# Performance work log

Hardware: AMD Instinct MI355X
Metric: run time of the kernel (lower is better)

Reference implementation:

```python
import jax, jax.numpy as jnp
import numpy as np

B, S, D, H, FF, L = 2, 2048, 512, 8, 2048, 2
HD = D // H
EPS = 1e-5
NEG = -1e9


def layernorm(x, gamma, beta):
    # mean/var over last axis (axis=2 in original)
    mean = jnp.mean(x, axis=-1, keepdims=True)
    var = jnp.mean((x - mean) ** 2, axis=-1, keepdims=True)
    return gamma * (x - mean) / jnp.sqrt(var + EPS) + beta


def masked_attention(x, mask, Wqkv, Wo, bo):
    b, s, d = x.shape
    qkv = x @ Wqkv                                  # [B,S,3D]
    qkv = qkv.reshape(b, s, H, 3 * HD)
    qkv = qkv.reshape(b, H, s, 3 * HD)              # original uses reshape, not transpose
    q, k, v = jnp.split(qkv, 3, axis=3)             # each [B,H,S,HD]
    scaled = jnp.einsum('bhqd,bhkd->bhqk', q, k) / (HD ** 0.5)
    col = mask[:, None, None, :]                    # valid key columns
    row = mask[:, None, :, None]                    # valid query rows
    logits = jnp.where(col, scaled, NEG)
    attn = jax.nn.softmax(logits, axis=-1)
    attn = attn * (row & col).astype(attn.dtype)    # exact zeros outside valid block
    values = jnp.einsum('bhqk,bhkd->bhqd', attn, v)  # [B,H,S,HD]
    values = values.reshape(b, s, H * HD)           # original uses reshape, not transpose
    return values @ Wo + bo


def encoder_layer(x, mask, p):
    res = x
    x = masked_attention(x, mask, p['Wqkv'], p['Wo'], p['bo'])
    x = layernorm(x + res, p['g1'], p['be1'])
    res = x
    x = jax.nn.relu(x @ p['W1'] + p['bf1']) @ p['W2'] + p['bf2']
    x = layernorm(x + res, p['g2'], p['be2'])
    return x


def setup_inputs() -> dict:
    key = jax.random.key(0)
    ks = jax.random.split(key, 8)
    x = jax.random.normal(ks[0], (B, S, D), jnp.float32)
    lengths = jax.random.randint(ks[1], (B,), S // 2, S + 1)
    paded_mask = jnp.arange(S)[None, :] < lengths[:, None]   # [B,S] bool
    sc = 0.02
    return {
        'x': x,
        'paded_mask': paded_mask,
        'Wqkv': jax.random.normal(ks[2], (L, D, 3 * D), jnp.float32) * sc,
        'Wo': jax.random.normal(ks[3], (L, D, D), jnp.float32) * sc,
        'bo': jnp.zeros((L, D), jnp.float32),
        'g1': jnp.ones((L, D), jnp.float32),
        'be1': jnp.zeros((L, D), jnp.float32),
        'W1': jax.random.normal(ks[4], (L, D, FF), jnp.float32) * sc,
        'bf1': jnp.zeros((L, FF), jnp.float32),
        'W2': jax.random.normal(ks[5], (L, FF, D), jnp.float32) * sc,
        'bf2': jnp.zeros((L, D), jnp.float32),
        'g2': jnp.ones((L, D), jnp.float32),
        'be2': jnp.zeros((L, D), jnp.float32),
    }


def reference(x, paded_mask, Wqkv, Wo, bo, g1, be1, W1, bf1, W2, bf2, g2, be2):
    for i in range(L):
        p = {'Wqkv': Wqkv[i], 'Wo': Wo[i], 'bo': bo[i], 'g1': g1[i], 'be1': be1[i],
             'W1': W1[i], 'bf1': bf1[i], 'W2': W2[i], 'bf2': bf2[i], 'g2': g2[i], 'be2': be2[i]}
        x = encoder_layer(x, paded_mask, p)
    return x
```

## Files before the change

kernel.cpp:

```cpp
#include <hip/hip_runtime.h>
#include <math.h>


typedef __bf16 bf16x8 __attribute__((ext_vector_type(8)));
typedef __bf16 bf16x4 __attribute__((ext_vector_type(4)));
typedef float f32x4 __attribute__((ext_vector_type(4)));

static constexpr int S_ = 2048;
static constexpr int D_ = 512;
static constexpr int FF_ = 2048;
static constexpr int M_ = 4096;
static constexpr int OPC_ = 2 * 8 * 2048;

#define GLDS16(gp, lp)                                                      \
  __builtin_amdgcn_global_load_lds(                                         \
      (const __attribute__((address_space(1))) void*)(gp),                  \
      (__attribute__((address_space(3))) void*)(lp), 16, 0, 0)

__global__ __launch_bounds__(256) void prep_kernel(
    const float* __restrict__ Wqkv, const float* __restrict__ Wo,
    const float* __restrict__ W1, const float* __restrict__ W2,
    const float* __restrict__ x,
    __bf16* __restrict__ WqkvT, __bf16* __restrict__ WoT,
    __bf16* __restrict__ W1T, __bf16* __restrict__ W2T,
    __bf16* __restrict__ x_bf) {
  __shared__ float tile[32][33];
  const int t = threadIdx.x;
  int bid = blockIdx.x;
  if (bid >= 6144) {
    const size_t i = ((size_t)(bid - 6144) * 256 + t) * 8;
    float4 f0 = *(const float4*)(x + i), f1 = *(const float4*)(x + i + 4);
    bf16x8 v;
    v[0] = (__bf16)f0.x; v[1] = (__bf16)f0.y; v[2] = (__bf16)f0.z; v[3] = (__bf16)f0.w;
    v[4] = (__bf16)f1.x; v[5] = (__bf16)f1.y; v[6] = (__bf16)f1.z; v[7] = (__bf16)f1.w;
    *(bf16x8*)(x_bf + i) = v;
    return;
  }
  const float* W;
  __bf16* Wt;
  int K, N;
  if (bid < 1536)      { W = Wqkv;              Wt = WqkvT; K = 512;  N = 1536; }
  else if (bid < 2048) { bid -= 1536; W = Wo;   Wt = WoT;   K = 512;  N = 512; }
  else if (bid < 4096) { bid -= 2048; W = W1;   Wt = W1T;   K = 512;  N = 2048; }
  else                 { bid -= 4096; W = W2;   Wt = W2T;   K = 2048; N = 512; }
  const int nx = N >> 5, ny = K >> 5;
  const int xb = bid % nx, yb = (bid / nx) % ny, l = bid / (nx * ny);
  const size_t off = (size_t)l * K * N;
  const int n0 = xb * 32, k0 = yb * 32;
  const int tx = t & 31, ty = t >> 5;
#pragma unroll
  for (int i = 0; i < 4; ++i)
    tile[ty + i * 8][tx] = W[off + (size_t)(k0 + ty + i * 8) * N + n0 + tx];
  __syncthreads();
#pragma unroll
  for (int i = 0; i < 4; ++i)
    Wt[off + (size_t)(n0 + ty + i * 8) * K + k0 + tx] = (__bf16)tile[tx][ty + i * 8];
}

template <int BN, bool RELU, bool SPLITK2, bool QKV, bool OUT_BF16>
__global__ __launch_bounds__(256) void gemm_async(
    const __bf16* __restrict__ A, const __bf16* __restrict__ Wt,
    const float* __restrict__ bias, void* __restrict__ Cv,
    __bf16* __restrict__ VT, int M, int N, int K) {
  constexpr int BM = 128, BK = 64;
  constexpr int MI = 4;
  constexpr int NJ = BN / 32;
  __shared__ __bf16 As[BM][BK];
  __shared__ __bf16 Bs[BN][BK];

  const int t = threadIdx.x;
  const int wv = t >> 6, ln = t & 63;
  const int ln16 = t & 15, quad = (t & 63) >> 4;
  const int bm = blockIdx.x * BM, bn = blockIdx.y * BN;
  const int wm = (wv & 1) * 64, wn = (wv >> 1) * (BN / 2);

  int kbeg = 0, kend = K;
  if (SPLITK2) {
    const int half = K >> 1;
    kbeg = blockIdx.z * half;
    kend = kbeg + half;
  }

  f32x4 acc[MI][NJ];
#pragma unroll
  for (int i = 0; i < MI; ++i)
#pragma unroll
    for (int j = 0; j < NJ; ++j) acc[i][j] = {0.f, 0.f, 0.f, 0.f};

  for (int k0 = kbeg; k0 < kend; k0 += BK) {
#pragma unroll
    for (int it = 0; it < 4; ++it) {
      const int cb = it * 256 + wv * 64;
      const int c = cb + ln;
      const int r = c >> 3, jl = (c & 7) ^ (r & 7);
      GLDS16(A + (size_t)(bm + r) * K + k0 + jl * 8,
             (char*)&As[0][0] + (size_t)cb * 16);
    }
#pragma unroll
    for (int it = 0; it < BN / 32; ++it) {
      const int cb = it * 256 + wv * 64;
      const int c = cb + ln;
      const int r = c >> 3, jl = (c & 7) ^ (r & 7);
      GLDS16(Wt + (size_t)(bn + r) * K + k0 + jl * 8,
             (char*)&Bs[0][0] + (size_t)cb * 16);
    }
    __syncthreads();

#pragma unroll
    for (int kk = 0; kk < 2; ++kk) {
      bf16x8 a[MI], b[NJ];
#pragma unroll
      for (int i = 0; i < MI; ++i) {
        const int r = wm + i * 16 + ln16;
        a[i] = *(const bf16x8*)&As[r][((kk * 4 + quad) ^ (r & 7)) * 8];
      }
#pragma unroll
      for (int j = 0; j < NJ; ++j) {
        const int r = wn + j * 16 + ln16;
        b[j] = *(const bf16x8*)&Bs[r][((kk * 4 + quad) ^ (r & 7)) * 8];
      }
#pragma unroll
      for (int i = 0; i < MI; ++i)
#pragma unroll
        for (int j = 0; j < NJ; ++j)
          acc[i][j] = __builtin_amdgcn_mfma_f32_16x16x32_bf16(a[i], b[j], acc[i][j], 0, 0, 0);
    }
    __syncthreads();
  }

  float* Cs = (float*)Cv;
  if (SPLITK2) Cs += (size_t)blockIdx.z * M * N;
  const bool addb = bias && (!SPLITK2 || blockIdx.z == 0);
  const int bidx = bm >> 11;
#pragma unroll
  for (int i = 0; i < MI; ++i) {
#pragma unroll
    for (int j = 0; j < NJ; ++j) {
      const int col = bn + wn + j * 16 + ln16;
      if (QKV && (col % 192) >= 128) {
        const int d = col % 192 - 128;
        const int n8 = col / 192;
#pragma unroll
        for (int r = 0; r < 4; ++r) {
          const int s = (bm + wm + i * 16 + quad * 4 + r) & 2047;
          const int h = s >> 8;
          const int s2 = ((s & 255) << 3) | n8;
          VT[(((size_t)(bidx * 8 + h) * 64 + d) << 11) + s2] = (__bf16)acc[i][j][r];
        }
      } else {
        const float bv = addb ? bias[col] : 0.f;
#pragma unroll
        for (int r = 0; r < 4; ++r) {
          const int row = bm + wm + i * 16 + quad * 4 + r;
          float v = acc[i][j][r] + bv;
          if (RELU) v = fmaxf(v, 0.f);
          if (OUT_BF16)
            ((__bf16*)Cv)[(size_t)row * N + col] = (__bf16)v;
          else
            Cs[(size_t)row * N + col] = v;
        }
      }
    }
  }
}

__global__ __launch_bounds__(256) void attn_mfma(
    const __bf16* __restrict__ qkv, const __bf16* __restrict__ VT,
    const int* __restrict__ mask, float* __restrict__ OP,
    float* __restrict__ LP) {
  const int b = blockIdx.z >> 1, chunk = blockIdx.z & 1;
  const int h = blockIdx.y;
  const int q0 = blockIdx.x * 64;
  const int t = threadIdx.x;
  const int wq = t >> 6, ln16 = t & 15, quad = (t & 63) >> 4;

  __shared__ __bf16 Ks[64][72];
  __shared__ __bf16 Vt[64][72];
  __shared__ __bf16 Ps[64][72];
  __shared__ int lred[4];
  __shared__ int len_sh;

  const __bf16* base = qkv + (size_t)b * S_ * 1536 + (size_t)h * S_ * 192;
  const __bf16* vbase = VT + ((size_t)(b * 8 + h) << 17);

  {
    int c = 0;
    const int* mp = mask + b * S_ + t * 8;
#pragma unroll
    for (int i = 0; i < 8; ++i) c += mp[i];
#pragma unroll
    for (int off = 32; off >= 1; off >>= 1) c += __shfl_down(c, off, 64);
    if ((t & 63) == 0) lred[t >> 6] = c;
  }
  __syncthreads();
  if (t == 0) len_sh = lred[0] + lred[1] + lred[2] + lred[3];
  __syncthreads();
  const int len = len_sh;

  if (q0 >= len) return;

  bf16x8 aq[2];
  {
    const int q = q0 + wq * 16 + ln16;
    aq[0] = *(const bf16x8*)(base + (size_t)q * 192 + quad * 8);
    aq[1] = *(const bf16x8*)(base + (size_t)q * 192 + 32 + quad * 8);
  }

  float lpart = 0.f;
  f32x4 o[4];
#pragma unroll
  for (int d = 0; d < 4; ++d) o[d] = {0.f, 0.f, 0.f, 0.f};

  const int kr = t >> 3, kc = (t & 7) * 8;
  const int vd = t >> 2, vc = (t & 3) * 16;
  const int vphys = vc ^ ((vd & 3) * 16);

  bf16x8 kreg[2], vreg[2];
  auto fetch = [&](int kt) {
    kreg[0] = *(const bf16x8*)(base + (size_t)(kt + kr) * 192 + 64 + kc);
    kreg[1] = *(const bf16x8*)(base + (size_t)(kt + kr + 32) * 192 + 64 + kc);
    const __bf16* vp = vbase + (size_t)vd * 2048 + kt + vc;
    vreg[0] = *(const bf16x8*)vp;
    vreg[1] = *(const bf16x8*)(vp + 8);
  };

  const int kbeg = chunk * 64;
  fetch(kbeg);

  for (int k0 = kbeg; k0 < len; k0 += 128) {
    *(bf16x8*)&Ks[kr][kc] = kreg[0];
    *(bf16x8*)&Ks[kr + 32][kc] = kreg[1];
    *(bf16x8*)&Vt[vd][vphys] = vreg[0];
    *(bf16x8*)&Vt[vd][vphys + 8] = vreg[1];
    __syncthreads();

    { const int kp = (k0 + 128 < S_) ? k0 + 128 : k0; fetch(kp); }

    f32x4 sf[4];
#pragma unroll
    for (int j = 0; j < 4; ++j) sf[j] = {0.f, 0.f, 0.f, 0.f};
#pragma unroll
    for (int kk = 0; kk < 2; ++kk) {
#pragma unroll
      for (int j = 0; j < 4; ++j) {
        bf16x8 ak = *(const bf16x8*)&Ks[j * 16 + ln16][kk * 32 + quad * 8];
        sf[j] = __builtin_amdgcn_mfma_f32_16x16x32_bf16(ak, aq[kk], sf[j], 0, 0, 0);
      }
    }

#pragma unroll
    for (int j = 0; j < 4; ++j) {
      bf16x4 pk;
#pragma unroll
      for (int r = 0; r < 4; ++r) {
        const float e = __expf(fminf(sf[j][r] * 0.125f, 60.f));
        const float p = (k0 + j * 16 + quad * 4 + r < len) ? e : 0.f;
        lpart += p;
        pk[r] = (__bf16)p;
      }
      *(bf16x4*)&Ps[wq * 16 + ln16][j * 16 + quad * 4] = pk;
    }
    asm volatile("s_waitcnt lgkmcnt(0)" ::: "memory");

#pragma unroll
    for (int kk = 0; kk < 2; ++kk) {
      bf16x8 pb = *(const bf16x8*)&Ps[wq * 16 + ln16][kk * 32 + quad * 8];
#pragma unroll
      for (int dt = 0; dt < 4; ++dt) {
        bf16x8 av = *(const bf16x8*)
            &Vt[dt * 16 + ln16][(kk * 32 + quad * 8) ^ ((ln16 & 3) * 16)];
        o[dt] = __builtin_amdgcn_mfma_f32_16x16x32_bf16(av, pb, o[dt], 0, 0, 0);
      }
    }
    __syncthreads();
  }

  lpart += __shfl_xor(lpart, 16, 64);
  lpart += __shfl_xor(lpart, 32, 64);

  const int q = q0 + wq * 16 + ln16;
  float* opc = OP + (size_t)chunk * OPC_ * 64 +
               ((size_t)((b * 8 + h) * 2048) + q) * 64;
#pragma unroll
  for (int dt = 0; dt < 4; ++dt)
    *(float4*)(opc + dt * 16 + quad * 4) =
        make_float4(o[dt][0], o[dt][1], o[dt][2], o[dt][3]);
  if (quad == 0) LP[chunk * OPC_ + (b * 8 + h) * 2048 + q] = lpart;
}

__global__ __launch_bounds__(256) void gemm_wo(
    const float* __restrict__ OP, const float* __restrict__ LP,
    const int* __restrict__ mask, const __bf16* __restrict__ Wt,
    const float* __restrict__ bias, float* __restrict__ C) {
  __shared__ __bf16 As[64][72];
  __shared__ __bf16 Bs[64][72];

  const int t = threadIdx.x;
  const int bm = blockIdx.x * 64, bn = blockIdx.y * 64;
  const int wv = t >> 6;
  const int ln16 = t & 15, quad = (t & 63) >> 4;
  const int wm = (wv & 1) * 32, wn = (wv >> 1) * 32;
  const int b = bm >> 11, qb = bm & 2047;
  const int sr = t >> 3, sc = (t & 7) * 8;

  const int mrow[2] = {mask[b * 2048 + qb + sr], mask[b * 2048 + qb + sr + 32]};

  f32x4 acc[2][2];
#pragma unroll
  for (int i = 0; i < 2; ++i)
#pragma unroll
    for (int j = 0; j < 2; ++j) acc[i][j] = {0.f, 0.f, 0.f, 0.f};

  bf16x8 avp[2], pbb[2];
  auto fetchA = [&](int h) {
    const float* O0 = OP + ((size_t)((b * 8 + h) * 2048) + qb) * 64;
#pragma unroll
    for (int it = 0; it < 2; ++it) {
      const int r = sr + it * 32;
      const int li = (b * 8 + h) * 2048 + qb + r;
      const float l = LP[li] + LP[OPC_ + li];
      const float s = (mrow[it] != 0 && l > 0.f) ? 1.f / l : 0.f;
      const float* p0 = O0 + (size_t)r * 64 + sc;
      const float* p1 = p0 + (size_t)OPC_ * 64;
      float4 a0 = *(const float4*)p0, a1 = *(const float4*)(p0 + 4);
      float4 b0 = *(const float4*)p1, b1 = *(const float4*)(p1 + 4);
      bf16x8 v;
      v[0] = (__bf16)((a0.x + b0.x) * s); v[1] = (__bf16)((a0.y + b0.y) * s);
      v[2] = (__bf16)((a0.z + b0.z) * s); v[3] = (__bf16)((a0.w + b0.w) * s);
      v[4] = (__bf16)((a1.x + b1.x) * s); v[5] = (__bf16)((a1.y + b1.y) * s);
      v[6] = (__bf16)((a1.z + b1.z) * s); v[7] = (__bf16)((a1.w + b1.w) * s);
      avp[it] = v;
    }
  };
  auto fetchB = [&](int k0) {
#pragma unroll
    for (int it = 0; it < 2; ++it)
      pbb[it] = *(const bf16x8*)(Wt + (size_t)(bn + sr + it * 32) * 512 + k0 + sc);
  };

  fetchA(0);
  fetchB(0);
  for (int h = 0; h < 8; ++h) {
    *(bf16x8*)&As[sr][sc] = avp[0];
    *(bf16x8*)&As[sr + 32][sc] = avp[1];
    *(bf16x8*)&Bs[sr][sc] = pbb[0];
    *(bf16x8*)&Bs[sr + 32][sc] = pbb[1];
    __syncthreads();
    if (h < 7) {
      fetchA(h + 1);
      fetchB((h + 1) * 64);
    }
#pragma unroll
    for (int kk = 0; kk < 2; ++kk) {
      bf16x8 a[2], bb[2];
#pragma unroll
      for (int i = 0; i < 2; ++i)
        a[i] = *(const bf16x8*)&As[wm + i * 16 + ln16][kk * 32 + quad * 8];
#pragma unroll
      for (int j = 0; j < 2; ++j)
        bb[j] = *(const bf16x8*)&Bs[wn + j * 16 + ln16][kk * 32 + quad * 8];
#pragma unroll
      for (int i = 0; i < 2; ++i)
#pragma unroll
        for (int j = 0; j < 2; ++j)
          acc[i][j] = __builtin_amdgcn_mfma_f32_16x16x32_bf16(a[i], bb[j], acc[i][j], 0, 0, 0);
    }
    __syncthreads();
  }

#pragma unroll
  for (int i = 0; i < 2; ++i) {
#pragma unroll
    for (int j = 0; j < 2; ++j) {
      const int col = bn + wn + j * 16 + ln16;
      const float bv = bias[col];
#pragma unroll
      for (int r = 0; r < 4; ++r) {
        const int row = bm + wm + i * 16 + quad * 4 + r;
        C[(size_t)row * 512 + col] = acc[i][j][r] + bv;
      }
    }
  }
}

__global__ __launch_bounds__(256) void add_ln_kernel(
    const float* __restrict__ a, const float* __restrict__ a2,
    const float* __restrict__ res, const float* __restrict__ g,
    const float* __restrict__ be, float* __restrict__ out,
    __bf16* __restrict__ out_bf) {
  const int row = blockIdx.x * 4 + (threadIdx.x >> 6);
  const int ln = threadIdx.x & 63;
  const int c = ln * 8;
  const float* pa = a + (size_t)row * D_ + c;
  const float* pr = res + (size_t)row * D_ + c;

  float4 v0 = *(const float4*)pa, v1 = *(const float4*)(pa + 4);
  float4 r0 = *(const float4*)pr, r1 = *(const float4*)(pr + 4);
  float w[8] = {v0.x + r0.x, v0.y + r0.y, v0.z + r0.z, v0.w + r0.w,
                v1.x + r1.x, v1.y + r1.y, v1.z + r1.z, v1.w + r1.w};
  if (a2) {
    const float* p2 = a2 + (size_t)row * D_ + c;
    float4 u0 = *(const float4*)p2, u1 = *(const float4*)(p2 + 4);
    w[0] += u0.x; w[1] += u0.y; w[2] += u0.z; w[3] += u0.w;
    w[4] += u1.x; w[5] += u1.y; w[6] += u1.z; w[7] += u1.w;
  }
  float s = 0.f, sq = 0.f;
#pragma unroll
  for (int e = 0; e < 8; ++e) {
    s += w[e];
    sq += w[e] * w[e];
  }
#pragma unroll
  for (int off = 1; off < 64; off <<= 1) {
    s += __shfl_xor(s, off, 64);
    sq += __shfl_xor(sq, off, 64);
  }
  const float mean = s * (1.0f / D_);
  const float var = sq * (1.0f / D_) - mean * mean;
  const float rstd = rsqrtf(var + 1e-5f);

  float4 g0 = *(const float4*)(g + c), g1 = *(const float4*)(g + c + 4);
  float4 b0 = *(const float4*)(be + c), b1 = *(const float4*)(be + c + 4);
  const float gv[8] = {g0.x, g0.y, g0.z, g0.w, g1.x, g1.y, g1.z, g1.w};
  const float bv[8] = {b0.x, b0.y, b0.z, b0.w, b1.x, b1.y, b1.z, b1.w};
  float y[8];
#pragma unroll
  for (int e = 0; e < 8; ++e) y[e] = gv[e] * (w[e] - mean) * rstd + bv[e];

  float* po = out + (size_t)row * D_ + c;
  *(float4*)po = make_float4(y[0], y[1], y[2], y[3]);
  *(float4*)(po + 4) = make_float4(y[4], y[5], y[6], y[7]);
  if (out_bf) {
    bf16x8 v;
#pragma unroll
    for (int e = 0; e < 8; ++e) v[e] = (__bf16)y[e];
    *(bf16x8*)(out_bf + (size_t)row * D_ + c) = v;
  }
}

extern "C" void kernel_launch(void* const* d_in, const int* in_sizes, int n_in,
                              void* d_out, int out_size, void* d_ws, size_t ws_size,
                              hipStream_t stream) {
  const float* x_in = (const float*)d_in[0];
  const int* mask   = (const int*)d_in[1];
  const float* Wqkv = (const float*)d_in[2];
  const float* Wo   = (const float*)d_in[3];
  const float* bo   = (const float*)d_in[4];
  const float* g1   = (const float*)d_in[5];
  const float* be1  = (const float*)d_in[6];
  const float* W1   = (const float*)d_in[7];
  const float* bf1  = (const float*)d_in[8];
  const float* W2   = (const float*)d_in[9];
  const float* bf2  = (const float*)d_in[10];
  const float* g2   = (const float*)d_in[11];
  const float* be2  = (const float*)d_in[12];
  float* out = (float*)d_out;

  char* w = (char*)d_ws;
  auto alloc = [&](size_t bytes) {
    char* p = w;
    w += (bytes + 255) & ~(size_t)255;
    return p;
  };
  __bf16* WqkvT = (__bf16*)alloc((size_t)2 * 512 * 1536 * 2);
  __bf16* WoT   = (__bf16*)alloc((size_t)2 * 512 * 512 * 2);
  __bf16* W1T   = (__bf16*)alloc((size_t)2 * 512 * 2048 * 2);
  __bf16* W2T   = (__bf16*)alloc((size_t)2 * 2048 * 512 * 2);
  __bf16* R1    = (__bf16*)alloc((size_t)M_ * FF_ * 2);
  __bf16* VTb   = (__bf16*)alloc((size_t)16 * 64 * 2048 * 2);
  float* R2     = (float*)alloc((size_t)2 * M_ * D_ * 4);
  float* proj   = (float*)alloc((size_t)M_ * D_ * 4);
  float* x1     = (float*)alloc((size_t)M_ * D_ * 4);
  float* xE     = (float*)alloc((size_t)M_ * D_ * 4);
  float* LP     = (float*)alloc((size_t)2 * OPC_ * 4);
  __bf16* x_bf  = (__bf16*)alloc((size_t)M_ * D_ * 2);
  __bf16* x1_bf = (__bf16*)alloc((size_t)M_ * D_ * 2);
  __bf16* xE_bf = (__bf16*)alloc((size_t)M_ * D_ * 2);

  prep_kernel<<<dim3(7168), 256, 0, stream>>>(Wqkv, Wo, W1, W2, x_in,
                                              WqkvT, WoT, W1T, W2T, x_bf);

  for (int l = 0; l < 2; ++l) {
    const float* xin = (l == 0) ? x_in : xE;
    const __bf16* xin_bf = (l == 0) ? x_bf : xE_bf;
    float* xout = (l == 1) ? out : xE;
    __bf16* xout_bf = (l == 0) ? xE_bf : nullptr;
    const __bf16* WqkvT_l = WqkvT + (size_t)l * 512 * 1536;
    const __bf16* WoT_l   = WoT + (size_t)l * 512 * 512;
    const __bf16* W1T_l   = W1T + (size_t)l * 512 * 2048;
    const __bf16* W2T_l   = W2T + (size_t)l * 2048 * 512;

    gemm_async<64, false, false, true, true><<<dim3(32, 24), 256, 0, stream>>>(
        xin_bf, WqkvT_l, nullptr, R1, VTb, M_, 1536, 512);
    attn_mfma<<<dim3(S_ / 64, 8, 4), 256, 0, stream>>>(R1, VTb, mask, R2, LP);
    gemm_wo<<<dim3(64, 8), 256, 0, stream>>>(R2, LP, mask, WoT_l,
                                             bo + (size_t)l * D_, proj);
    add_ln_kernel<<<dim3(M_ / 4), 256, 0, stream>>>(proj, nullptr, xin,
                                                    g1 + (size_t)l * D_,
                                                    be1 + (size_t)l * D_, x1, x1_bf);
    gemm_async<128, true, false, false, true><<<dim3(32, 16), 256, 0, stream>>>(
        x1_bf, W1T_l, bf1 + (size_t)l * FF_, R1, nullptr, M_, 2048, 512);
    gemm_async<64, false, true, false, false><<<dim3(32, 8, 2), 256, 0, stream>>>(
        R1, W2T_l, bf2 + (size_t)l * D_, R2, nullptr, M_, 512, 2048);
    add_ln_kernel<<<dim3(M_ / 4), 256, 0, stream>>>(R2, R2 + (size_t)M_ * D_, x1,
                                                    g2 + (size_t)l * D_,
                                                    be2 + (size_t)l * D_, xout, xout_bf);
  }
}
```

Measured before the change: 346.6 us.

## Load K fragments directly into registers and double-buffer V tile in LDS

Attention kernel now loads K MFMA operands straight from global memory into registers instead of staging them through shared memory, and double-buffers the V tile in LDS so the trailing barrier per iteration can be dropped. This is meant to cut LDS traffic and one __syncthreads per key tile, overlapping the QK^T MFMAs with the V store. In exchange it uses more registers (8 bf16x8 K fragments prefetched) and issues uncoalesced per-lane global loads for K, which may raise memory latency or reduce occupancy.

New measurement: 405.9 us. 1.17x slower.

```diff
diff --git a/kernel.cpp b/kernel.cpp
--- a/kernel.cpp
+++ b/kernel.cpp
@@ -174,8 +174,7 @@
   const int t = threadIdx.x;
   const int wq = t >> 6, ln16 = t & 15, quad = (t & 63) >> 4;
 
-  __shared__ __bf16 Ks[64][72];
-  __shared__ __bf16 Vt[64][72];
+  __shared__ __bf16 Vt[2][64][72];
   __shared__ __bf16 Ps[64][72];
   __shared__ int lred[4];
   __shared__ int len_sh;
@@ -211,41 +210,47 @@
 #pragma unroll
   for (int d = 0; d < 4; ++d) o[d] = {0.f, 0.f, 0.f, 0.f};
 
-  const int kr = t >> 3, kc = (t & 7) * 8;
   const int vd = t >> 2, vc = (t & 3) * 16;
   const int vphys = vc ^ ((vd & 3) * 16);
 
-  bf16x8 kreg[2], vreg[2];
-  auto fetch = [&](int kt) {
-    kreg[0] = *(const bf16x8*)(base + (size_t)(kt + kr) * 192 + 64 + kc);
-    kreg[1] = *(const bf16x8*)(base + (size_t)(kt + kr + 32) * 192 + 64 + kc);
+  bf16x8 akn[2][4], vreg[2];
+  auto fetchK = [&](int kt) {
+#pragma unroll
+    for (int kk = 0; kk < 2; ++kk)
+#pragma unroll
+      for (int j = 0; j < 4; ++j)
+        akn[kk][j] = *(const bf16x8*)(base +
+            (size_t)(kt + j * 16 + ln16) * 192 + 64 + kk * 32 + quad * 8);
+  };
+  auto fetchV = [&](int kt) {
     const __bf16* vp = vbase + (size_t)vd * 2048 + kt + vc;
     vreg[0] = *(const bf16x8*)vp;
     vreg[1] = *(const bf16x8*)(vp + 8);
   };
 
   const int kbeg = chunk * 64;
-  fetch(kbeg);
-
+  fetchK(kbeg);
+  fetchV(kbeg);
+
+  int p = 0;
   for (int k0 = kbeg; k0 < len; k0 += 128) {
-    *(bf16x8*)&Ks[kr][kc] = kreg[0];
-    *(bf16x8*)&Ks[kr + 32][kc] = kreg[1];
-    *(bf16x8*)&Vt[vd][vphys] = vreg[0];
-    *(bf16x8*)&Vt[vd][vphys + 8] = vreg[1];
+    f32x4 sf[4];
+#pragma unroll
+    for (int j = 0; j < 4; ++j) sf[j] = {0.f, 0.f, 0.f, 0.f};
+#pragma unroll
+    for (int kk = 0; kk < 2; ++kk)
+#pragma unroll
+      for (int j = 0; j < 4; ++j)
+        sf[j] = __builtin_amdgcn_mfma_f32_16x16x32_bf16(akn[kk][j], aq[kk], sf[j], 0, 0, 0);
+
+    *(bf16x8*)&Vt[p][vd][vphys] = vreg[0];
+    *(bf16x8*)&Vt[p][vd][vphys + 8] = vreg[1];
     __syncthreads();
 
-    { const int kp = (k0 + 128 < S_) ? k0 + 128 : k0; fetch(kp); }
-
-    f32x4 sf[4];
-#pragma unroll
-    for (int j = 0; j < 4; ++j) sf[j] = {0.f, 0.f, 0.f, 0.f};
-#pragma unroll
-    for (int kk = 0; kk < 2; ++kk) {
-#pragma unroll
-      for (int j = 0; j < 4; ++j) {
-        bf16x8 ak = *(const bf16x8*)&Ks[j * 16 + ln16][kk * 32 + quad * 8];
-        sf[j] = __builtin_amdgcn_mfma_f32_16x16x32_bf16(ak, aq[kk], sf[j], 0, 0, 0);
-      }
+    {
+      const int kp = (k0 + 128 < S_) ? k0 + 128 : k0;
+      fetchK(kp);
+      fetchV(kp);
     }
 
 #pragma unroll
@@ -254,9 +259,9 @@
 #pragma unroll
       for (int r = 0; r < 4; ++r) {
         const float e = __expf(fminf(sf[j][r] * 0.125f, 60.f));
-        const float p = (k0 + j * 16 + quad * 4 + r < len) ? e : 0.f;
-        lpart += p;
-        pk[r] = (__bf16)p;
+        const float pv = (k0 + j * 16 + quad * 4 + r < len) ? e : 0.f;
+        lpart += pv;
+        pk[r] = (__bf16)pv;
       }
       *(bf16x4*)&Ps[wq * 16 + ln16][j * 16 + quad * 4] = pk;
     }
@@ -268,11 +273,11 @@
 #pragma unroll
       for (int dt = 0; dt < 4; ++dt) {
         bf16x8 av = *(const bf16x8*)
-            &Vt[dt * 16 + ln16][(kk * 32 + quad * 8) ^ ((ln16 & 3) * 16)];
+            &Vt[p][dt * 16 + ln16][(kk * 32 + quad * 8) ^ ((ln16 & 3) * 16)];
         o[dt] = __builtin_amdgcn_mfma_f32_16x16x32_bf16(av, pb, o[dt], 0, 0, 0);
       }
     }
-    __syncthreads();
+    p ^= 1;
   }
 
   lpart += __shfl_xor(lpart, 16, 64);
```
